# Kernel optimization log

Hardware: AMD Instinct MI355X
Metric: run time of the kernel (lower is better)

Reference implementation:

```python
import jax, jax.numpy as jnp
import numpy as np

B, T, I, H = 32, 2048, 512, 512


def setup_inputs() -> dict:
    key = jax.random.key(0)
    ks = jax.random.split(key, 5)
    s_ih = 1.0 / np.sqrt(H)
    return {
        "x_t": jax.random.normal(ks[0], (B, T, I), dtype=jnp.float32),
        # PyTorch LSTM params, gate order [i, f, g, o]
        "W_ih": jax.random.uniform(ks[1], (4 * H, I), minval=-s_ih, maxval=s_ih, dtype=jnp.float32),
        "W_hh": jax.random.uniform(ks[2], (4 * H, H), minval=-s_ih, maxval=s_ih, dtype=jnp.float32),
        "b_ih": jax.random.uniform(ks[3], (4 * H,), minval=-s_ih, maxval=s_ih, dtype=jnp.float32),
        "b_hh": jax.random.uniform(ks[4], (4 * H,), minval=-s_ih, maxval=s_ih, dtype=jnp.float32),
    }


def _lstm_last_h(x_t, W_ih, W_hh, b_ih, b_hh):
    Bx = x_t.shape[0]
    Hh = W_hh.shape[1]
    # Precompute input projections for all timesteps in one big GEMM: [B,T,4H]
    x_proj = jnp.einsum("bti,gi->btg", x_t, W_ih) + (b_ih + b_hh)

    def step(carry, xp_t):
        h, c = carry
        z = xp_t + h @ W_hh.T  # [B, 4H]
        i, f, g, o = jnp.split(z, 4, axis=-1)
        i = jax.nn.sigmoid(i)
        f = jax.nn.sigmoid(f)
        g = jnp.tanh(g)
        o = jax.nn.sigmoid(o)
        c = f * c + i * g
        h = o * jnp.tanh(c)
        return (h, c), None

    h0 = jnp.zeros((Bx, Hh), dtype=x_t.dtype)
    c0 = jnp.zeros((Bx, Hh), dtype=x_t.dtype)
    (h_T, _), _ = jax.lax.scan(step, (h0, c0), jnp.swapaxes(x_proj, 0, 1))
    return h_T[None, :, :]  # [1, B, H] to match torch (num_layers*dirs, B, H)


def reference(x_t, W_ih, W_hh, b_ih, b_hh):
    return _lstm_last_h(x_t, W_ih, W_hh, b_ih, b_hh)
```

## Files before the change

### kernel.cpp

```cpp
#include <hip/hip_runtime.h>


#define T_FULL 2048
#define CHUNK  128
#define NCHUNK 16
#define NBLK   32
#define NGEMM  224

typedef float  f32x4 __attribute__((ext_vector_type(4)));
typedef short  s16x8 __attribute__((ext_vector_type(8)));
typedef unsigned int u32;

#define MFMA16(a,b,c) __builtin_amdgcn_mfma_f32_16x16x32_bf16((a),(b),(c),0,0,0)

__device__ inline unsigned short f2bf(float f){
  unsigned u = __builtin_bit_cast(unsigned, f);
  u += 0x7fffu + ((u>>16)&1u);
  return (unsigned short)(u>>16);
}
__device__ inline float bf2f(unsigned short s){
  unsigned u = ((unsigned)s)<<16;
  return __builtin_bit_cast(float, u);
}
__device__ inline float sigmoid_(float x){
  x = fminf(fmaxf(x,-30.f),30.f);
  return 1.f/(1.f + __expf(-x));
}
__device__ inline float tanh_(float x){
  x = fminf(fmaxf(x,-15.f),15.f);
  float e = __expf(2.f*x);
  return (e-1.f)/(e+1.f);
}

__device__ void gemm_tile(const float* __restrict__ x, const float* __restrict__ Wih,
                          const float* __restrict__ bih, const float* __restrict__ bhh,
                          unsigned short* __restrict__ xp, int t0, int nx, int ny,
                          char* smem)
{
  unsigned short* At = (unsigned short*)smem;
  unsigned short* Bt = (unsigned short*)(smem + 17408);
  const int tid = threadIdx.x, lane = tid&63, w = tid>>6;
  const int l15 = lane&15, l4 = lane>>4;
  const int n0 = nx*64, m0 = ny*64;
  const int mbase = (w&1)*32, nbase = (w>>1)*32;

  f32x4 acc[2][2];
  #pragma unroll
  for (int mi=0; mi<2; ++mi)
    #pragma unroll
    for (int ni=0; ni<2; ++ni)
      acc[mi][ni] = (f32x4){0.f,0.f,0.f,0.f};

  for (int kb=0; kb<4; ++kb){
    #pragma unroll
    for (int it=0; it<4; ++it){
      int grp = it*256 + tid;
      int row = grp>>4, c8 = (grp&15)*8;
      {
        int m = m0 + row;
        size_t t = (size_t)t0 + (m>>5), b = (size_t)(m&31);
        const float* src = x + ((b*2048 + t)<<9) + kb*128 + c8;
        f32x4 v0 = *(const f32x4*)src, v1 = *(const f32x4*)(src+4);
        unsigned short* d = &At[row*136 + c8];
        d[0]=f2bf(v0[0]); d[1]=f2bf(v0[1]); d[2]=f2bf(v0[2]); d[3]=f2bf(v0[3]);
        d[4]=f2bf(v1[0]); d[5]=f2bf(v1[1]); d[6]=f2bf(v1[2]); d[7]=f2bf(v1[3]);
      }
      {
        const float* src = Wih + (size_t)(n0+row)*512 + kb*128 + c8;
        f32x4 v0 = *(const f32x4*)src, v1 = *(const f32x4*)(src+4);
        unsigned short* d = &Bt[row*136 + c8];
        d[0]=f2bf(v0[0]); d[1]=f2bf(v0[1]); d[2]=f2bf(v0[2]); d[3]=f2bf(v0[3]);
        d[4]=f2bf(v1[0]); d[5]=f2bf(v1[1]); d[6]=f2bf(v1[2]); d[7]=f2bf(v1[3]);
      }
    }
    __syncthreads();
    #pragma unroll
    for (int ks=0; ks<4; ++ks){
      s16x8 af0 = *(const s16x8*)&At[(mbase+   l15)*136 + ks*32 + l4*8];
      s16x8 af1 = *(const s16x8*)&At[(mbase+16+l15)*136 + ks*32 + l4*8];
      s16x8 bf0 = *(const s16x8*)&Bt[(nbase+   l15)*136 + ks*32 + l4*8];
      s16x8 bf1 = *(const s16x8*)&Bt[(nbase+16+l15)*136 + ks*32 + l4*8];
      acc[0][0] = MFMA16(af0,bf0,acc[0][0]);
      acc[0][1] = MFMA16(af0,bf1,acc[0][1]);
      acc[1][0] = MFMA16(af1,bf0,acc[1][0]);
      acc[1][1] = MFMA16(af1,bf1,acc[1][1]);
    }
    __syncthreads();
  }
  #pragma unroll
  for (int ni=0; ni<2; ++ni){
    int col = n0 + nbase + ni*16 + l15;
    float bias = bih[col] + bhh[col];
    #pragma unroll
    for (int mi=0; mi<2; ++mi){
      #pragma unroll
      for (int r=0; r<4; ++r){
        int mrow = m0 + mbase + mi*16 + l4*4 + r;
        xp[(size_t)mrow*2048 + col] = f2bf(acc[mi][ni][r] + bias);
      }
    }
  }
}

__global__ __launch_bounds__(256) void lstm_p1(
    const float* __restrict__ x, const float* __restrict__ Wih,
    const float* __restrict__ bih, const float* __restrict__ bhh,
    unsigned short* __restrict__ xp, int t0)
{
  __shared__ __align__(16) char smem[34816];
  gemm_tile(x, Wih, bih, bhh, xp, t0, blockIdx.x, blockIdx.y, smem);
}

__global__ __launch_bounds__(256,1) void lstm_fused(
    const unsigned short* __restrict__ xp_cur,
    const float* __restrict__ x, const float* __restrict__ Wih,
    const float* __restrict__ bih, const float* __restrict__ bhh,
    unsigned short* __restrict__ xp_next, const float* __restrict__ Whh,
    unsigned short* __restrict__ Hbuf, float* __restrict__ cst,
    u32* __restrict__ flag, float* __restrict__ out, int t0, int do_gemm)
{
  __shared__ __align__(16) char smem[41472];
  const int bid = blockIdx.x;

  if (bid >= NBLK){
    if (do_gemm){
      const int t0n = t0 + CHUNK;
      for (int tile = bid - NBLK; tile < 32*(CHUNK*32/64); tile += NGEMM)
        gemm_tile(x, Wih, bih, bhh, xp_next, t0n, tile & 31, tile >> 5, smem);
    }
    return;
  }

  char* Hl = smem;
  float (*zl)[68] = (float(*)[68])(smem + 32768);
  const int k = bid;
  const int tid = threadIdx.x;
  const int lane = tid & 63, w = tid >> 6;
  const int l15 = lane & 15, l4 = lane >> 4;
  const int mt = w & 1, gp = w >> 1;

  s16x8 wf[2][16];
  #pragma unroll
  for (int nt=0; nt<2; ++nt){
    int lrow = gp*32 + nt*16 + l15;
    int grow = (lrow>>4)*512 + k*16 + (lrow&15);
    const float* wr = Whh + (size_t)grow*512;
    #pragma unroll
    for (int ks=0; ks<16; ++ks){
      const float* s = wr + ks*32 + l4*8;
      f32x4 v0 = *(const f32x4*)s, v1 = *(const f32x4*)(s+4);
      s16x8 tv;
      tv[0]=(short)f2bf(v0[0]); tv[1]=(short)f2bf(v0[1]);
      tv[2]=(short)f2bf(v0[2]); tv[3]=(short)f2bf(v0[3]);
      tv[4]=(short)f2bf(v1[0]); tv[5]=(short)f2bf(v1[1]);
      tv[6]=(short)f2bf(v1[2]); tv[7]=(short)f2bf(v1[3]);
      wf[nt][ks] = tv;
    }
  }

  const int s_ = tid >> 3, a_ = tid & 7;
  const int ucol = k*16 + 2*a_;
  float c0 = cst[s_*512 + ucol], c1 = cst[s_*512 + ucol + 1];

  #define PLOAD() ((lane < NBLK) \
      ? __hip_atomic_load(&flag[lane<<5], __ATOMIC_RELAXED, __HIP_MEMORY_SCOPE_AGENT) \
      : 0xffffffffu)

  for (int tt=0; tt<CHUNK; ++tt){
    const int t = t0 + tt;

    unsigned int xq[4];
    #pragma unroll
    for (int g=0; g<4; ++g)
      xq[g] = *(const unsigned int*)(xp_cur + (size_t)(tt*32 + s_)*2048 + g*512 + ucol);

    if (t > 0){
      if (w == 0){
        u32 va = PLOAD();
        u32 vb = PLOAD();
        u32 vc = PLOAD();
        for (;;){
          u32 vd = PLOAD();
          if (__all(va >= (u32)t)) break;
          va = PLOAD();
          if (__all(vb >= (u32)t)) break;
          vb = PLOAD();
          if (__all(vc >= (u32)t)) break;
          vc = PLOAD();
          if (__all(vd >= (u32)t)) break;
        }
        __builtin_amdgcn_fence(__ATOMIC_ACQUIRE, "agent");
      }
      __syncthreads();
    }

    {
      const char* hsrc = (const char*)(Hbuf + ((t+1)&1)*(32*512));
      #pragma unroll
      for (int it=0; it<8; ++it){
        int off = (it*256 + tid)*16;
        f32x4 v = *(const f32x4*)(hsrc + off);
        *(f32x4*)&Hl[off ^ (((off>>10)&7)<<4)] = v;
      }
    }
    __syncthreads();

    f32x4 acc0 = (f32x4){0.f,0.f,0.f,0.f};
    f32x4 acc1 = (f32x4){0.f,0.f,0.f,0.f};
    {
      const int row = mt*16 + l15;
      const int swz = (row&7)<<4;
      const int rbase = row<<10;
      #pragma unroll
      for (int ks=0; ks<16; ++ks){
        int cb = ks*64 + l4*16;
        s16x8 af = *(const s16x8*)&Hl[rbase | (cb ^ swz)];
        acc0 = MFMA16(af, wf[0][ks], acc0);
        acc1 = MFMA16(af, wf[1][ks], acc1);
      }
    }
    #pragma unroll
    for (int r=0; r<4; ++r){
      zl[mt*16 + l4*4 + r][gp*32 +      l15] = acc0[r];
      zl[mt*16 + l4*4 + r][gp*32 + 16 + l15] = acc1[r];
    }
    __syncthreads();

    float zi0 = zl[s_][ 0 + 2*a_    ] + bf2f((unsigned short)(xq[0]&0xffffu));
    float zi1 = zl[s_][ 0 + 2*a_ + 1] + bf2f((unsigned short)(xq[0]>>16));
    float zf0 = zl[s_][16 + 2*a_    ] + bf2f((unsigned short)(xq[1]&0xffffu));
    float zf1 = zl[s_][16 + 2*a_ + 1] + bf2f((unsigned short)(xq[1]>>16));
    float zg0 = zl[s_][32 + 2*a_    ] + bf2f((unsigned short)(xq[2]&0xffffu));
    float zg1 = zl[s_][32 + 2*a_ + 1] + bf2f((unsigned short)(xq[2]>>16));
    float zo0 = zl[s_][48 + 2*a_    ] + bf2f((unsigned short)(xq[3]&0xffffu));
    float zo1 = zl[s_][48 + 2*a_ + 1] + bf2f((unsigned short)(xq[3]>>16));

    float i0 = sigmoid_(zi0), f0 = sigmoid_(zf0), g0 = tanh_(zg0), o0 = sigmoid_(zo0);
    float i1 = sigmoid_(zi1), f1 = sigmoid_(zf1), g1 = tanh_(zg1), o1 = sigmoid_(zo1);
    c0 = f0*c0 + i0*g0;
    c1 = f1*c1 + i1*g1;
    float h0 = o0 * tanh_(c0);
    float h1 = o1 * tanh_(c1);

    {
      unsigned short* hdst = Hbuf + (t&1)*(32*512);
      unsigned int hp = (unsigned int)f2bf(h0) | ((unsigned int)f2bf(h1)<<16);
      __hip_atomic_store((unsigned int*)((char*)hdst + s_*1024 + ucol*2), hp,
                         __ATOMIC_RELAXED, __HIP_MEMORY_SCOPE_AGENT);
    }
    if (t == T_FULL-1){
      out[s_*512 + ucol    ] = h0;
      out[s_*512 + ucol + 1] = h1;
    }

    asm volatile("s_waitcnt vmcnt(0)" ::: "memory");
    __syncthreads();
    if (tid == 0)
      __hip_atomic_store(&flag[k<<5], (unsigned)(t+1),
                         __ATOMIC_RELAXED, __HIP_MEMORY_SCOPE_AGENT);
  }

  #undef PLOAD

  cst[s_*512 + ucol    ] = c0;
  cst[s_*512 + ucol + 1] = c1;
}

extern "C" void kernel_launch(void* const* d_in, const int* in_sizes, int n_in,
                              void* d_out, int out_size, void* d_ws, size_t ws_size,
                              hipStream_t stream)
{
  const float* x   = (const float*)d_in[0];
  const float* Wih = (const float*)d_in[1];
  const float* Whh = (const float*)d_in[2];
  const float* bih = (const float*)d_in[3];
  const float* bhh = (const float*)d_in[4];
  float* out = (float*)d_out;

  char* ws = (char*)d_ws;
  const size_t XPB = (size_t)CHUNK*32*2048*2;
  unsigned short* xp0  = (unsigned short*)ws;
  unsigned short* xp1  = (unsigned short*)(ws + XPB);
  unsigned short* Hbuf = (unsigned short*)(ws + 2*XPB);
  float*          cst  = (float*)(ws + 2*XPB + 65536);
  u32*            flag = (u32*)(ws + 2*XPB + 65536 + 65536);

  (void)hipMemsetAsync(Hbuf, 0, 65536 + 65536 + 4096, stream);

  lstm_p1<<<dim3(32, CHUNK*32/64), 256, 0, stream>>>(x, Wih, bih, bhh, xp0, 0);

  for (int c=0; c<NCHUNK; ++c){
    unsigned short* xc = (c & 1) ? xp1 : xp0;
    unsigned short* xn = (c & 1) ? xp0 : xp1;
    lstm_fused<<<256, 256, 0, stream>>>(xc, x, Wih, bih, bhh, xn, Whh,
                                        Hbuf, cst, flag, out, c*CHUNK,
                                        (c < NCHUNK-1) ? 1 : 0);
  }
}
```

Measured before the change: 6.185 ms.

## Halve recurrent blocks to 16 with 512-thread blocks owning 32 hidden units

The recurrent phase now runs on 16 blocks of 512 threads instead of 32 blocks of 256. Each block owns 32 hidden units, with each wave holding one 16-column W_hh tile and computing both batch halves. Fewer blocks take part in the per-timestep flag barrier, so polling cost and cross-block synchronisation latency should drop. The GEMM side gains blocks, but only 4 of its 8 waves compute. Per-block recurrent work doubles, which may lengthen each step's critical path.

```diff
diff --git a/kernel.cpp b/kernel.cpp
--- a/kernel.cpp
+++ b/kernel.cpp
@@ -4,8 +4,8 @@
 #define T_FULL 2048
 #define CHUNK  128
 #define NCHUNK 16
-#define NBLK   32
-#define NGEMM  224
+#define NBLK   16
+#define NGEMM  240
 
 typedef float  f32x4 __attribute__((ext_vector_type(4)));
 typedef short  s16x8 __attribute__((ext_vector_type(8)));
@@ -42,7 +42,7 @@
   const int tid = threadIdx.x, lane = tid&63, w = tid>>6;
   const int l15 = lane&15, l4 = lane>>4;
   const int n0 = nx*64, m0 = ny*64;
-  const int mbase = (w&1)*32, nbase = (w>>1)*32;
+  const int mbase = (w&1)*32, nbase = ((w>>1)&1)*32;
 
   f32x4 acc[2][2];
   #pragma unroll
@@ -53,8 +53,8 @@
 
   for (int kb=0; kb<4; ++kb){
     #pragma unroll
-    for (int it=0; it<4; ++it){
-      int grp = it*256 + tid;
+    for (int it=0; it<2; ++it){
+      int grp = it*512 + tid;
       int row = grp>>4, c8 = (grp&15)*8;
       {
         int m = m0 + row;
@@ -74,35 +74,39 @@
       }
     }
     __syncthreads();
-    #pragma unroll
-    for (int ks=0; ks<4; ++ks){
-      s16x8 af0 = *(const s16x8*)&At[(mbase+   l15)*136 + ks*32 + l4*8];
-      s16x8 af1 = *(const s16x8*)&At[(mbase+16+l15)*136 + ks*32 + l4*8];
-      s16x8 bf0 = *(const s16x8*)&Bt[(nbase+   l15)*136 + ks*32 + l4*8];
-      s16x8 bf1 = *(const s16x8*)&Bt[(nbase+16+l15)*136 + ks*32 + l4*8];
-      acc[0][0] = MFMA16(af0,bf0,acc[0][0]);
-      acc[0][1] = MFMA16(af0,bf1,acc[0][1]);
-      acc[1][0] = MFMA16(af1,bf0,acc[1][0]);
-      acc[1][1] = MFMA16(af1,bf1,acc[1][1]);
-    }
-    __syncthreads();
-  }
-  #pragma unroll
-  for (int ni=0; ni<2; ++ni){
-    int col = n0 + nbase + ni*16 + l15;
-    float bias = bih[col] + bhh[col];
-    #pragma unroll
-    for (int mi=0; mi<2; ++mi){
-      #pragma unroll
-      for (int r=0; r<4; ++r){
-        int mrow = m0 + mbase + mi*16 + l4*4 + r;
-        xp[(size_t)mrow*2048 + col] = f2bf(acc[mi][ni][r] + bias);
-      }
-    }
-  }
-}
-
-__global__ __launch_bounds__(256) void lstm_p1(
+    if (w < 4){
+      #pragma unroll
+      for (int ks=0; ks<4; ++ks){
+        s16x8 af0 = *(const s16x8*)&At[(mbase+   l15)*136 + ks*32 + l4*8];
+        s16x8 af1 = *(const s16x8*)&At[(mbase+16+l15)*136 + ks*32 + l4*8];
+        s16x8 bf0 = *(const s16x8*)&Bt[(nbase+   l15)*136 + ks*32 + l4*8];
+        s16x8 bf1 = *(const s16x8*)&Bt[(nbase+16+l15)*136 + ks*32 + l4*8];
+        acc[0][0] = MFMA16(af0,bf0,acc[0][0]);
+        acc[0][1] = MFMA16(af0,bf1,acc[0][1]);
+        acc[1][0] = MFMA16(af1,bf0,acc[1][0]);
+        acc[1][1] = MFMA16(af1,bf1,acc[1][1]);
+      }
+    }
+    __syncthreads();
+  }
+  if (w < 4){
+    #pragma unroll
+    for (int ni=0; ni<2; ++ni){
+      int col = n0 + nbase + ni*16 + l15;
+      float bias = bih[col] + bhh[col];
+      #pragma unroll
+      for (int mi=0; mi<2; ++mi){
+        #pragma unroll
+        for (int r=0; r<4; ++r){
+          int mrow = m0 + mbase + mi*16 + l4*4 + r;
+          xp[(size_t)mrow*2048 + col] = f2bf(acc[mi][ni][r] + bias);
+        }
+      }
+    }
+  }
+}
+
+__global__ __launch_bounds__(512) void lstm_p1(
     const float* __restrict__ x, const float* __restrict__ Wih,
     const float* __restrict__ bih, const float* __restrict__ bhh,
     unsigned short* __restrict__ xp, int t0)
@@ -111,7 +115,7 @@
   gemm_tile(x, Wih, bih, bhh, xp, t0, blockIdx.x, blockIdx.y, smem);
 }
 
-__global__ __launch_bounds__(256,1) void lstm_fused(
+__global__ __launch_bounds__(512,1) void lstm_fused(
     const unsigned short* __restrict__ xp_cur,
     const float* __restrict__ x, const float* __restrict__ Wih,
     const float* __restrict__ bih, const float* __restrict__ bhh,
@@ -119,7 +123,7 @@
     unsigned short* __restrict__ Hbuf, float* __restrict__ cst,
     u32* __restrict__ flag, float* __restrict__ out, int t0, int do_gemm)
 {
-  __shared__ __align__(16) char smem[41472];
+  __shared__ __align__(16) char smem[49664];
   const int bid = blockIdx.x;
 
   if (bid >= NBLK){
@@ -132,18 +136,16 @@
   }
 
   char* Hl = smem;
-  float (*zl)[68] = (float(*)[68])(smem + 32768);
+  float (*zl)[132] = (float(*)[132])(smem + 32768);
   const int k = bid;
   const int tid = threadIdx.x;
   const int lane = tid & 63, w = tid >> 6;
   const int l15 = lane & 15, l4 = lane >> 4;
-  const int mt = w & 1, gp = w >> 1;
-
-  s16x8 wf[2][16];
-  #pragma unroll
-  for (int nt=0; nt<2; ++nt){
-    int lrow = gp*32 + nt*16 + l15;
-    int grow = (lrow>>4)*512 + k*16 + (lrow&15);
+
+  s16x8 wf[16];
+  {
+    const int lrow = w*16 + l15;
+    const int grow = (lrow>>5)*512 + k*32 + (lrow&31);
     const float* wr = Whh + (size_t)grow*512;
     #pragma unroll
     for (int ks=0; ks<16; ++ks){
@@ -154,12 +156,13 @@
       tv[2]=(short)f2bf(v0[2]); tv[3]=(short)f2bf(v0[3]);
       tv[4]=(short)f2bf(v1[0]); tv[5]=(short)f2bf(v1[1]);
       tv[6]=(short)f2bf(v1[2]); tv[7]=(short)f2bf(v1[3]);
-      wf[nt][ks] = tv;
-    }
-  }
-
-  const int s_ = tid >> 3, a_ = tid & 7;
-  const int ucol = k*16 + 2*a_;
+      wf[ks] = tv;
+    }
+  }
+
+  const int s_ = tid >> 4;
+  const int a_ = tid & 15;
+  const int ucol = k*32 + 2*a_;
   float c0 = cst[s_*512 + ucol], c1 = cst[s_*512 + ucol + 1];
 
   #define PLOAD() ((lane < NBLK) \
@@ -177,17 +180,11 @@
     if (t > 0){
       if (w == 0){
         u32 va = PLOAD();
-        u32 vb = PLOAD();
-        u32 vc = PLOAD();
         for (;;){
-          u32 vd = PLOAD();
+          u32 vb = PLOAD();
           if (__all(va >= (u32)t)) break;
           va = PLOAD();
           if (__all(vb >= (u32)t)) break;
-          vb = PLOAD();
-          if (__all(vc >= (u32)t)) break;
-          vc = PLOAD();
-          if (__all(vd >= (u32)t)) break;
         }
         __builtin_amdgcn_fence(__ATOMIC_ACQUIRE, "agent");
       }
@@ -197,8 +194,8 @@
     {
       const char* hsrc = (const char*)(Hbuf + ((t+1)&1)*(32*512));
       #pragma unroll
-      for (int it=0; it<8; ++it){
-        int off = (it*256 + tid)*16;
+      for (int it=0; it<4; ++it){
+        int off = (it*512 + tid)*16;
         f32x4 v = *(const f32x4*)(hsrc + off);
         *(f32x4*)&Hl[off ^ (((off>>10)&7)<<4)] = v;
       }
@@ -208,32 +205,32 @@
     f32x4 acc0 = (f32x4){0.f,0.f,0.f,0.f};
     f32x4 acc1 = (f32x4){0.f,0.f,0.f,0.f};
     {
-      const int row = mt*16 + l15;
-      const int swz = (row&7)<<4;
-      const int rbase = row<<10;
+      const int swz = (l15&7)<<4;
+      const int rb0 = l15<<10, rb1 = (16+l15)<<10;
       #pragma unroll
       for (int ks=0; ks<16; ++ks){
         int cb = ks*64 + l4*16;
-        s16x8 af = *(const s16x8*)&Hl[rbase | (cb ^ swz)];
-        acc0 = MFMA16(af, wf[0][ks], acc0);
-        acc1 = MFMA16(af, wf[1][ks], acc1);
+        s16x8 af0 = *(const s16x8*)&Hl[rb0 | (cb ^ swz)];
+        s16x8 af1 = *(const s16x8*)&Hl[rb1 | (cb ^ swz)];
+        acc0 = MFMA16(af0, wf[ks], acc0);
+        acc1 = MFMA16(af1, wf[ks], acc1);
       }
     }
     #pragma unroll
     for (int r=0; r<4; ++r){
-      zl[mt*16 + l4*4 + r][gp*32 +      l15] = acc0[r];
-      zl[mt*16 + l4*4 + r][gp*32 + 16 + l15] = acc1[r];
-    }
-    __syncthreads();
-
-    float zi0 = zl[s_][ 0 + 2*a_    ] + bf2f((unsigned short)(xq[0]&0xffffu));
-    float zi1 = zl[s_][ 0 + 2*a_ + 1] + bf2f((unsigned short)(xq[0]>>16));
-    float zf0 = zl[s_][16 + 2*a_    ] + bf2f((unsigned short)(xq[1]&0xffffu));
-    float zf1 = zl[s_][16 + 2*a_ + 1] + bf2f((unsigned short)(xq[1]>>16));
-    float zg0 = zl[s_][32 + 2*a_    ] + bf2f((unsigned short)(xq[2]&0xffffu));
-    float zg1 = zl[s_][32 + 2*a_ + 1] + bf2f((unsigned short)(xq[2]>>16));
-    float zo0 = zl[s_][48 + 2*a_    ] + bf2f((unsigned short)(xq[3]&0xffffu));
-    float zo1 = zl[s_][48 + 2*a_ + 1] + bf2f((unsigned short)(xq[3]>>16));
+      zl[     l4*4 + r][w*16 + l15] = acc0[r];
+      zl[16 + l4*4 + r][w*16 + l15] = acc1[r];
+    }
+    __syncthreads();
+
+    float zi0 = zl[s_][  0 + 2*a_    ] + bf2f((unsigned short)(xq[0]&0xffffu));
+    float zi1 = zl[s_][  0 + 2*a_ + 1] + bf2f((unsigned short)(xq[0]>>16));
+    float zf0 = zl[s_][ 32 + 2*a_    ] + bf2f((unsigned short)(xq[1]&0xffffu));
+    float zf1 = zl[s_][ 32 + 2*a_ + 1] + bf2f((unsigned short)(xq[1]>>16));
+    float zg0 = zl[s_][ 64 + 2*a_    ] + bf2f((unsigned short)(xq[2]&0xffffu));
+    float zg1 = zl[s_][ 64 + 2*a_ + 1] + bf2f((unsigned short)(xq[2]>>16));
+    float zo0 = zl[s_][ 96 + 2*a_    ] + bf2f((unsigned short)(xq[3]&0xffffu));
+    float zo1 = zl[s_][ 96 + 2*a_ + 1] + bf2f((unsigned short)(xq[3]>>16));
 
     float i0 = sigmoid_(zi0), f0 = sigmoid_(zf0), g0 = tanh_(zg0), o0 = sigmoid_(zo0);
     float i1 = sigmoid_(zi1), f1 = sigmoid_(zf1), g1 = tanh_(zg1), o1 = sigmoid_(zo1);
@@ -287,12 +284,12 @@
 
   (void)hipMemsetAsync(Hbuf, 0, 65536 + 65536 + 4096, stream);
 
-  lstm_p1<<<dim3(32, CHUNK*32/64), 256, 0, stream>>>(x, Wih, bih, bhh, xp0, 0);
+  lstm_p1<<<dim3(32, CHUNK*32/64), 512, 0, stream>>>(x, Wih, bih, bhh, xp0, 0);
 
   for (int c=0; c<NCHUNK; ++c){
     unsigned short* xc = (c & 1) ? xp1 : xp0;
     unsigned short* xn = (c & 1) ? xp0 : xp1;
-    lstm_fused<<<256, 256, 0, stream>>>(xc, x, Wih, bih, bhh, xn, Whh,
+    lstm_fused<<<256, 512, 0, stream>>>(xc, x, Wih, bih, bhh, xn, Whh,
                                         Hbuf, cst, flag, out, c*CHUNK,
                                         (c < NCHUNK-1) ? 1 : 0);
   }
```

After: 7.528 ms. 21.7% more time.
